# Performance work log

Measured on AMD Instinct MI355X. Metric: run time of the kernel, lower is better.

The kernel has to match this reference:

```python
import jax, jax.numpy as jnp
import numpy as np

D_MODEL = 1024
NUM_HEADS = 16
D_HEAD = D_MODEL // NUM_HEADS
B, S = 2, 2048


def setup_inputs() -> dict:
    key = jax.random.key(0)
    ks = jax.random.split(key, 12)
    s = 0.02
    return {
        "query": jax.random.normal(ks[0], (B, S, D_MODEL), jnp.float32),
        "key": jax.random.normal(ks[1], (B, S, D_MODEL), jnp.float32),
        "value": jax.random.normal(ks[2], (B, S, D_MODEL), jnp.float32),
        "mask": jnp.ones((B, 1, 1, S), jnp.float32),
        "W_q": jax.random.normal(ks[3], (D_MODEL, D_MODEL), jnp.float32) * s,
        "b_q": jnp.zeros((D_MODEL,), jnp.float32),
        "W_k": jax.random.normal(ks[4], (D_MODEL, D_MODEL), jnp.float32) * s,
        "b_k": jnp.zeros((D_MODEL,), jnp.float32),
        "W_v": jax.random.normal(ks[5], (D_MODEL, D_MODEL), jnp.float32) * s,
        "b_v": jnp.zeros((D_MODEL,), jnp.float32),
        "W_o": jax.random.normal(ks[6], (D_MODEL, D_MODEL), jnp.float32) * s,
        "b_o": jnp.zeros((D_MODEL,), jnp.float32),
    }


def reference(query, key, value, mask, W_q, b_q, W_k, b_k, W_v, b_v, W_o, b_o):
    # Linear projections (torch nn.Linear: x @ W.T + b; here W stored as [in, out])
    q = query @ W_q + b_q
    k = key @ W_k + b_k
    v = value @ W_v + b_v
    # [B, S, D] -> [B, H, S, Dh]
    def split_heads(x):
        b, s, _ = x.shape
        return x.reshape(b, s, NUM_HEADS, D_HEAD).transpose(0, 2, 1, 3)
    q, k, v = split_heads(q), split_heads(k), split_heads(v)
    # scaled dot-product attention; full [B,H,Sq,Sk] matrix (faithful to source)
    logits = jnp.einsum("bhqd,bhkd->bhqk", q, k) / jnp.sqrt(jnp.float32(D_HEAD))
    logits = logits + (1.0 - mask) * (-1e9)
    attn = jax.nn.softmax(logits, axis=-1)
    # dropout is identity in eval mode
    ctx = jnp.einsum("bhqk,bhkd->bhqd", attn, v)
    ctx = ctx.transpose(0, 2, 1, 3).reshape(ctx.shape[0], -1, D_MODEL)
    out = ctx @ W_o + b_o
    return out, attn
```

## Files before the change

kernel.cpp:

```cpp
#include <hip/hip_runtime.h>
#include <hip/hip_bf16.h>

#define BATCH 2
#define SEQ 2048
#define DM 1024
#define NH 16
#define DH 64
#define MTOT (BATCH*SEQ)

typedef __attribute__((ext_vector_type(8))) short bf16x8;
typedef __attribute__((ext_vector_type(4))) float f32x4;
typedef __attribute__((ext_vector_type(16))) float f32x16;
typedef __attribute__((ext_vector_type(4))) float float4v;
typedef __attribute__((ext_vector_type(8))) unsigned short u16x8;
typedef __attribute__((ext_vector_type(4))) unsigned short u16x4;

#define GLDS16(g, l) __builtin_amdgcn_global_load_lds(                         \
    (const __attribute__((address_space(1))) void*)(g),                        \
    (__attribute__((address_space(3))) void*)(l), 16, 0, 0)

static __device__ __forceinline__ float bf2f(unsigned short u) {
    unsigned int x = ((unsigned int)u) << 16;
    float f; __builtin_memcpy(&f, &x, 4); return f;
}
static __device__ __forceinline__ unsigned short f2bf(float f) {
    unsigned int x; __builtin_memcpy(&x, &f, 4);
    x += 0x7fffu + ((x >> 16) & 1);
    return (unsigned short)(x >> 16);
}
static __device__ __forceinline__ unsigned int cvt_pk_bf16(float a, float b) {
    unsigned int r;
    asm volatile("v_cvt_pk_bf16_f32 %0, %1, %2" : "=v"(r) : "v"(a), "v"(b));
    return r;
}

__global__ __launch_bounds__(256) void cvt_kernel(
    const float* __restrict__ q, const float* __restrict__ k, const float* __restrict__ v,
    unsigned short* __restrict__ oq, unsigned short* __restrict__ ok_, unsigned short* __restrict__ ov) {
    const float* in = blockIdx.y == 0 ? q : (blockIdx.y == 1 ? k : v);
    unsigned short* out = blockIdx.y == 0 ? oq : (blockIdx.y == 1 ? ok_ : ov);
    size_t i = ((size_t)blockIdx.x * 256 + threadIdx.x) * 8;
    float4v a = *(const float4v*)(in + i);
    float4v b = *(const float4v*)(in + i + 4);
    u16x8 r;
    r[0]=f2bf(a[0]); r[1]=f2bf(a[1]); r[2]=f2bf(a[2]); r[3]=f2bf(a[3]);
    r[4]=f2bf(b[0]); r[5]=f2bf(b[1]); r[6]=f2bf(b[2]); r[7]=f2bf(b[3]);
    *(u16x8*)(out + i) = r;
}

__global__ __launch_bounds__(256) void wtrans_kernel(
    const float* __restrict__ w0, const float* __restrict__ w1,
    const float* __restrict__ w2, const float* __restrict__ w3,
    unsigned short* __restrict__ t0, unsigned short* __restrict__ t1,
    unsigned short* __restrict__ t2, unsigned short* __restrict__ t3) {
    const float* w = blockIdx.z==0 ? w0 : blockIdx.z==1 ? w1 : blockIdx.z==2 ? w2 : w3;
    unsigned short* wt = blockIdx.z==0 ? t0 : blockIdx.z==1 ? t1 : blockIdx.z==2 ? t2 : t3;
    __shared__ float tile[64][65];
    const int t = threadIdx.x;
    const int k0 = blockIdx.x * 64, n0 = blockIdx.y * 64;
    const int tr = t >> 4, tc = t & 15;
#pragma unroll
    for (int i = 0; i < 4; ++i) {
        float4v val = *(const float4v*)(w + (size_t)(k0 + tr + 16*i) * DM + n0 + tc*4);
        tile[tr + 16*i][tc*4 + 0] = val[0];
        tile[tr + 16*i][tc*4 + 1] = val[1];
        tile[tr + 16*i][tc*4 + 2] = val[2];
        tile[tr + 16*i][tc*4 + 3] = val[3];
    }
    __syncthreads();
#pragma unroll
    for (int i = 0; i < 4; ++i) {
        u16x4 o;
#pragma unroll
        for (int j = 0; j < 4; ++j) o[j] = f2bf(tile[tc*4 + j][tr + 16*i]);
        *(u16x4*)(wt + (size_t)(n0 + tr + 16*i) * DM + k0 + tc*4) = o;
    }
}

__global__ __launch_bounds__(256) void vtrans_kernel(
    const unsigned short* __restrict__ vws, unsigned short* __restrict__ vtg) {
    __shared__ unsigned short tile[64][72];
    const int t = threadIdx.x;
    const int bh = blockIdx.y, b = bh >> 4, h = bh & 15;
    const int k0 = blockIdx.x * 64;
#pragma unroll
    for (int i = 0; i < 2; ++i) {
        int u = i*256 + t;
        int key = u >> 3, dc = (u & 7) * 8;
        u16x8 v = *(const u16x8*)(vws + (size_t)(b*SEQ + k0 + key)*DM + h*DH + dc);
#pragma unroll
        for (int j = 0; j < 8; ++j) tile[dc + j][key] = v[j];
    }
    __syncthreads();
#pragma unroll
    for (int i = 0; i < 2; ++i) {
        int u = i*256 + t;
        int d = u >> 3, kc = (u & 7) * 8;
        u16x8 o;
#pragma unroll
        for (int j = 0; j < 8; ++j) o[j] = tile[d][kc + j];
        *(u16x8*)(vtg + ((size_t)bh*DH + d)*SEQ + k0 + kc) = o;
    }
}

template<int OUTMODE>
static __device__ __forceinline__ void gemm_body(
    const unsigned short* __restrict__ A, const unsigned short* __restrict__ Bt,
    const float* __restrict__ bias, void* __restrict__ Cout,
    unsigned short* a_lds, unsigned short* b_lds) {
    constexpr int BM = 128, BN = 64, BK = 64, NT = DM / BK;
    const int tid = threadIdx.x;
    const int m0 = blockIdx.y * BM, n0 = blockIdx.x * BN;
    const int w = tid >> 6, l = tid & 63;
    const int lr = l & 15, lg = l >> 4;
    const int wm = (w >> 1) * 64, wn = (w & 1) * 32;
    f32x4 acc[4][2] = {};

    auto stage = [&](int buf, int kt) {
        const int k0 = kt * BK;
#pragma unroll
        for (int i = 0; i < 4; ++i) {
            int u = i*256 + tid;
            int row = u >> 3, slot = u & 7;
            int sc = (slot ^ (row & 7)) * 8;
            GLDS16(A + (size_t)(m0 + row)*DM + k0 + sc, a_lds + buf*BM*BK + u*8);
        }
#pragma unroll
        for (int i = 0; i < 2; ++i) {
            int u = i*256 + tid;
            int row = u >> 3, slot = u & 7;
            int sc = (slot ^ (row & 7)) * 8;
            GLDS16(Bt + (size_t)(n0 + row)*DM + k0 + sc, b_lds + buf*BN*BK + u*8);
        }
    };

    stage(0, 0);
    for (int kt = 0; kt < NT; ++kt) {
        __syncthreads();
        if (kt < NT-1) stage((kt+1)&1, kt+1);
        const char* ab = (const char*)(a_lds + (kt&1)*BM*BK);
        const char* bb = (const char*)(b_lds + (kt&1)*BN*BK);
        bf16x8 af[4][2], bfr[2][2];
#pragma unroll
        for (int r = 0; r < 4; ++r)
#pragma unroll
            for (int kc = 0; kc < 2; ++kc) {
                int row = wm + r*16 + lr;
                af[r][kc] = *(const bf16x8*)(ab + row*128 + ((kc*64 + lg*16) ^ ((row&7)<<4)));
            }
#pragma unroll
        for (int c = 0; c < 2; ++c)
#pragma unroll
            for (int kc = 0; kc < 2; ++kc) {
                int row = wn + c*16 + lr;
                bfr[c][kc] = *(const bf16x8*)(bb + row*128 + ((kc*64 + lg*16) ^ ((row&7)<<4)));
            }
#pragma unroll
        for (int r = 0; r < 4; ++r)
#pragma unroll
            for (int c = 0; c < 2; ++c)
#pragma unroll
                for (int kc = 0; kc < 2; ++kc)
                    acc[r][c] = __builtin_amdgcn_mfma_f32_16x16x32_bf16(af[r][kc], bfr[c][kc], acc[r][c], 0, 0, 0);
    }

#pragma unroll
    for (int r = 0; r < 4; ++r)
#pragma unroll
        for (int c = 0; c < 2; ++c) {
            int m = m0 + wm + r*16 + lg*4;
            int n = n0 + wn + c*16 + lr;
            float bb = bias[n];
            if constexpr (OUTMODE == 1) {
                float* o = (float*)Cout;
#pragma unroll
                for (int j = 0; j < 4; ++j) o[(size_t)(m+j)*DM + n] = acc[r][c][j] + bb;
            } else {
                unsigned short* o = (unsigned short*)Cout;
#pragma unroll
                for (int j = 0; j < 4; ++j) o[(size_t)(m+j)*DM + n] = f2bf(acc[r][c][j] + bb);
            }
        }
}

__global__ __launch_bounds__(256) void gemm_qkv_kernel(
    const unsigned short* __restrict__ A0, const unsigned short* __restrict__ A1, const unsigned short* __restrict__ A2,
    const unsigned short* __restrict__ B0, const unsigned short* __restrict__ B1, const unsigned short* __restrict__ B2,
    const float* __restrict__ c0, const float* __restrict__ c1, const float* __restrict__ c2,
    unsigned short* __restrict__ O0, unsigned short* __restrict__ O1, unsigned short* __restrict__ O2) {
    __shared__ __align__(16) unsigned short smem[2*128*64 + 2*64*64];
    const int z = blockIdx.z;
    const unsigned short* A = z==0 ? A0 : z==1 ? A1 : A2;
    const unsigned short* B = z==0 ? B0 : z==1 ? B1 : B2;
    const float* c = z==0 ? c0 : z==1 ? c1 : c2;
    unsigned short* O = z==0 ? O0 : z==1 ? O1 : O2;
    gemm_body<0>(A, B, c, O, smem, smem + 2*128*64);
}

__global__ __launch_bounds__(256) void gemm_out_kernel(
    const unsigned short* __restrict__ A, const unsigned short* __restrict__ Bt,
    const float* __restrict__ bias, float* __restrict__ Cout) {
    __shared__ __align__(16) unsigned short smem[2*128*64 + 2*64*64];
    gemm_body<1>(A, Bt, bias, Cout, smem, smem + 2*128*64);
}

__global__ __launch_bounds__(256) void attn_kernel(
    const unsigned short* __restrict__ qw, const unsigned short* __restrict__ kw,
    const unsigned short* __restrict__ vtg, const float* __restrict__ mask,
    float* __restrict__ attn_out, unsigned short* __restrict__ ctx) {
    constexpr int QB = 128, KB = 64, NT = SEQ / KB;
    __shared__ __align__(16) unsigned short smem[2*KB*DH + 2*KB*DH];
    unsigned short* kbuf = smem;
    unsigned short* vbuf = smem + 2*KB*DH;
    const int tid = threadIdx.x, w = tid >> 6, l = tid & 63;
    const int q32 = l & 31, hi = l >> 5;
    const int u0 = (blockIdx.x & 7) * 64 + (blockIdx.x >> 3);
    const int qblk = u0 & 15, bh = u0 >> 4;
    const int b = bh >> 4, h = bh & 15;
    const int q0 = qblk * QB;
    const int q = q0 + w*32 + q32;

    bf16x8 qf[4];
    {
        const unsigned short* qp = qw + ((size_t)(b*SEQ + q))*DM + h*DH + hi*8;
#pragma unroll
        for (int ks = 0; ks < 4; ++ks) {
            bf16x8 t = *(const bf16x8*)(qp + ks*16);
#pragma unroll
            for (int j = 0; j < 8; ++j) t[j] = (short)f2bf(bf2f((unsigned short)t[j]) * 0.125f);
            qf[ks] = t;
        }
    }

    auto stageK = [&](int buf, int kt) {
        const unsigned short* base = kw + ((size_t)(b*SEQ + kt*KB))*DM + h*DH;
#pragma unroll
        for (int i = 0; i < 2; ++i) {
            int uu = i*256 + tid;
            int row = uu >> 3, slot = uu & 7;
            int sc = (slot ^ (row & 7)) * 8;
            GLDS16(base + (size_t)row*DM + sc, kbuf + buf*KB*DH + uu*8);
        }
    };
    auto stageV = [&](int buf, int kt) {
        const unsigned short* base = vtg + ((size_t)bh*DH)*SEQ + (size_t)kt*KB;
#pragma unroll
        for (int i = 0; i < 2; ++i) {
            int uu = i*256 + tid;
            int row = uu >> 3, slot = uu & 7;
            int sc = (slot ^ (row & 7)) * 8;
            GLDS16(base + (size_t)row*SEQ + sc, vbuf + buf*KB*DH + uu*8);
        }
    };

    const float* mrow = mask + (size_t)b*SEQ;

    float rs = 0.f;
    stageK(0, 0);
    for (int kt = 0; kt < NT; ++kt) {
        __syncthreads();
        if (kt < NT-1) stageK((kt+1)&1, kt+1);
        const char* kb = (const char*)(kbuf + (kt&1)*KB*DH);
#pragma unroll
        for (int sub = 0; sub < 2; ++sub) {
            f32x16 s = {};
#pragma unroll
            for (int ks = 0; ks < 4; ++ks) {
                int key = sub*32 + q32;
                bf16x8 kf = *(const bf16x8*)(kb + key*128 + ((ks*32 + hi*16) ^ ((key&7)<<4)));
                s = __builtin_amdgcn_mfma_f32_32x32x16_bf16(kf, qf[ks], s, 0, 0, 0);
            }
#pragma unroll
            for (int rq = 0; rq < 4; ++rq) {
                float4v m4 = *(const float4v*)(mrow + kt*KB + sub*32 + rq*8 + hi*4);
#pragma unroll
                for (int r = 0; r < 4; ++r)
                    rs += __expf(s[rq*4 + r] + (1.0f - m4[r]) * (-1e9f));
            }
        }
    }
    rs += __shfl_xor(rs, 32);
    const float rinv = 1.0f / rs;

    f32x16 oacc[2] = {};
    float* attn_row = attn_out + ((size_t)bh*SEQ + q)*SEQ;
    stageK(0, 0); stageV(0, 0);
    for (int kt = 0; kt < NT; ++kt) {
        __syncthreads();
        if (kt < NT-1) { stageK((kt+1)&1, kt+1); stageV((kt+1)&1, kt+1); }
        const char* kb = (const char*)(kbuf + (kt&1)*KB*DH);
        const char* vb = (const char*)(vbuf + (kt&1)*KB*DH);
#pragma unroll
        for (int sub = 0; sub < 2; ++sub) {
            f32x16 s = {};
#pragma unroll
            for (int ks = 0; ks < 4; ++ks) {
                int key = sub*32 + q32;
                bf16x8 kf = *(const bf16x8*)(kb + key*128 + ((ks*32 + hi*16) ^ ((key&7)<<4)));
                s = __builtin_amdgcn_mfma_f32_32x32x16_bf16(kf, qf[ks], s, 0, 0, 0);
            }
            float p[16];
#pragma unroll
            for (int rq = 0; rq < 4; ++rq) {
                float4v m4 = *(const float4v*)(mrow + kt*KB + sub*32 + rq*8 + hi*4);
                float4v pv;
#pragma unroll
                for (int r = 0; r < 4; ++r) {
                    pv[r] = __expf(s[rq*4 + r] + (1.0f - m4[r]) * (-1e9f)) * rinv;
                    p[rq*4 + r] = pv[r];
                }
                *(float4v*)(attn_row + kt*KB + sub*32 + rq*8 + hi*4) = pv;
            }
#pragma unroll
            for (int half = 0; half < 2; ++half) {
                unsigned int w0 = cvt_pk_bf16(p[half*8+0], p[half*8+1]);
                unsigned int w1 = cvt_pk_bf16(p[half*8+2], p[half*8+3]);
                unsigned int w2 = cvt_pk_bf16(p[half*8+4], p[half*8+5]);
                unsigned int w3 = cvt_pk_bf16(p[half*8+6], p[half*8+7]);
                asm volatile("v_permlane32_swap_b32 %0, %1" : "+v"(w0), "+v"(w2));
                asm volatile("v_permlane32_swap_b32 %0, %1" : "+v"(w1), "+v"(w3));
                union { unsigned int uu[4]; bf16x8 v; } pa;
                pa.uu[0] = w0; pa.uu[1] = w1; pa.uu[2] = w2; pa.uu[3] = w3;
                const int ks4 = sub*2 + half;
#pragma unroll
                for (int dsub = 0; dsub < 2; ++dsub) {
                    int d = dsub*32 + q32;
                    bf16x8 vf = *(const bf16x8*)(vb + d*128 + ((ks4*32 + hi*16) ^ ((d&7)<<4)));
                    oacc[dsub] = __builtin_amdgcn_mfma_f32_32x32x16_bf16(pa.v, vf, oacc[dsub], 0, 0, 0);
                }
            }
        }
    }
#pragma unroll
    for (int dsub = 0; dsub < 2; ++dsub) {
        int d = h*DH + dsub*32 + q32;
#pragma unroll
        for (int reg = 0; reg < 16; ++reg) {
            int qr = q0 + w*32 + (reg&3) + 8*(reg>>2) + 4*hi;
            ctx[(size_t)(b*SEQ + qr)*DM + d] = f2bf(oacc[dsub][reg]);
        }
    }
}

extern "C" void kernel_launch(void* const* d_in, const int* in_sizes, int n_in,
                              void* d_out, int out_size, void* d_ws, size_t ws_size,
                              hipStream_t stream) {
    const float* query = (const float*)d_in[0];
    const float* key_  = (const float*)d_in[1];
    const float* value = (const float*)d_in[2];
    const float* mask  = (const float*)d_in[3];
    const float* W_q = (const float*)d_in[4];
    const float* b_q = (const float*)d_in[5];
    const float* W_k = (const float*)d_in[6];
    const float* b_k = (const float*)d_in[7];
    const float* W_v = (const float*)d_in[8];
    const float* b_v = (const float*)d_in[9];
    const float* W_o = (const float*)d_in[10];
    const float* b_o = (const float*)d_in[11];

    char* ws = (char*)d_ws;
    const size_t SZ = (size_t)MTOT * DM * 2;
    unsigned short* xq  = (unsigned short*)(ws);
    unsigned short* xk  = (unsigned short*)(ws + SZ);
    unsigned short* xv  = (unsigned short*)(ws + 2*SZ);
    unsigned short* wtq = (unsigned short*)(ws + 3*SZ);
    unsigned short* wtk = wtq + (size_t)DM*DM;
    unsigned short* wtv = wtk + (size_t)DM*DM;
    unsigned short* wto = wtv + (size_t)DM*DM;
    unsigned short* qws = (unsigned short*)(ws + 4*SZ);
    unsigned short* kws = (unsigned short*)(ws + 5*SZ);
    unsigned short* vws = (unsigned short*)(ws + 6*SZ);
    unsigned short* ctx = (unsigned short*)(ws + 7*SZ);
    unsigned short* vtg = xq;
    float* out_f  = (float*)d_out;
    float* attn_f = out_f + (size_t)MTOT * DM;

    cvt_kernel<<<dim3(MTOT*DM/(256*8), 3), 256, 0, stream>>>(query, key_, value, xq, xk, xv);
    wtrans_kernel<<<dim3(16, 16, 4), 256, 0, stream>>>(W_q, W_k, W_v, W_o, wtq, wtk, wtv, wto);
    gemm_qkv_kernel<<<dim3(16, 32, 3), 256, 0, stream>>>(xq, xk, xv, wtq, wtk, wtv,
                                                         b_q, b_k, b_v, qws, kws, vws);
    vtrans_kernel<<<dim3(SEQ/64, BATCH*NH), 256, 0, stream>>>(vws, vtg);
    attn_kernel<<<dim3(512), 256, 0, stream>>>(qws, kws, vtg, mask, attn_f, ctx);
    gemm_out_kernel<<<dim3(16, 32), 256, 0, stream>>>(ctx, wto, b_o, out_f);
}
```

Measured before the change: 305.0 us.

## Merge prep kernels, fuse V transpose into GEMM, split-K attention across warps

Merges the input conversion and weight transpose into one prep kernel. The V projection GEMM now writes its output directly in transposed per-head layout, which removes the separate vtrans pass. GEMM tiles grow from 128x64 to 128x128. The attention kernel doubles its threads to 512 so two warp groups each handle half of the key range, then combine row sums and context partials through shared memory. The aim is fewer launches, less memory traffic and more parallelism per block, at the cost of extra barriers and scattered 8-byte transposed stores.

```diff
diff --git a/kernel.cpp b/kernel.cpp
--- a/kernel.cpp
+++ b/kernel.cpp
@@ -34,72 +34,49 @@
     return r;
 }
 
-__global__ __launch_bounds__(256) void cvt_kernel(
+__global__ __launch_bounds__(256) void prep_kernel(
     const float* __restrict__ q, const float* __restrict__ k, const float* __restrict__ v,
-    unsigned short* __restrict__ oq, unsigned short* __restrict__ ok_, unsigned short* __restrict__ ov) {
-    const float* in = blockIdx.y == 0 ? q : (blockIdx.y == 1 ? k : v);
-    unsigned short* out = blockIdx.y == 0 ? oq : (blockIdx.y == 1 ? ok_ : ov);
-    size_t i = ((size_t)blockIdx.x * 256 + threadIdx.x) * 8;
-    float4v a = *(const float4v*)(in + i);
-    float4v b = *(const float4v*)(in + i + 4);
-    u16x8 r;
-    r[0]=f2bf(a[0]); r[1]=f2bf(a[1]); r[2]=f2bf(a[2]); r[3]=f2bf(a[3]);
-    r[4]=f2bf(b[0]); r[5]=f2bf(b[1]); r[6]=f2bf(b[2]); r[7]=f2bf(b[3]);
-    *(u16x8*)(out + i) = r;
-}
-
-__global__ __launch_bounds__(256) void wtrans_kernel(
+    unsigned short* __restrict__ oq, unsigned short* __restrict__ ok_, unsigned short* __restrict__ ov,
     const float* __restrict__ w0, const float* __restrict__ w1,
     const float* __restrict__ w2, const float* __restrict__ w3,
     unsigned short* __restrict__ t0, unsigned short* __restrict__ t1,
     unsigned short* __restrict__ t2, unsigned short* __restrict__ t3) {
-    const float* w = blockIdx.z==0 ? w0 : blockIdx.z==1 ? w1 : blockIdx.z==2 ? w2 : w3;
-    unsigned short* wt = blockIdx.z==0 ? t0 : blockIdx.z==1 ? t1 : blockIdx.z==2 ? t2 : t3;
     __shared__ float tile[64][65];
-    const int t = threadIdx.x;
-    const int k0 = blockIdx.x * 64, n0 = blockIdx.y * 64;
-    const int tr = t >> 4, tc = t & 15;
-#pragma unroll
-    for (int i = 0; i < 4; ++i) {
-        float4v val = *(const float4v*)(w + (size_t)(k0 + tr + 16*i) * DM + n0 + tc*4);
-        tile[tr + 16*i][tc*4 + 0] = val[0];
-        tile[tr + 16*i][tc*4 + 1] = val[1];
-        tile[tr + 16*i][tc*4 + 2] = val[2];
-        tile[tr + 16*i][tc*4 + 3] = val[3];
-    }
-    __syncthreads();
-#pragma unroll
-    for (int i = 0; i < 4; ++i) {
-        u16x4 o;
-#pragma unroll
-        for (int j = 0; j < 4; ++j) o[j] = f2bf(tile[tc*4 + j][tr + 16*i]);
-        *(u16x4*)(wt + (size_t)(n0 + tr + 16*i) * DM + k0 + tc*4) = o;
-    }
-}
-
-__global__ __launch_bounds__(256) void vtrans_kernel(
-    const unsigned short* __restrict__ vws, unsigned short* __restrict__ vtg) {
-    __shared__ unsigned short tile[64][72];
-    const int t = threadIdx.x;
-    const int bh = blockIdx.y, b = bh >> 4, h = bh & 15;
-    const int k0 = blockIdx.x * 64;
-#pragma unroll
-    for (int i = 0; i < 2; ++i) {
-        int u = i*256 + t;
-        int key = u >> 3, dc = (u & 7) * 8;
-        u16x8 v = *(const u16x8*)(vws + (size_t)(b*SEQ + k0 + key)*DM + h*DH + dc);
-#pragma unroll
-        for (int j = 0; j < 8; ++j) tile[dc + j][key] = v[j];
-    }
-    __syncthreads();
-#pragma unroll
-    for (int i = 0; i < 2; ++i) {
-        int u = i*256 + t;
-        int d = u >> 3, kc = (u & 7) * 8;
-        u16x8 o;
-#pragma unroll
-        for (int j = 0; j < 8; ++j) o[j] = tile[d][kc + j];
-        *(u16x8*)(vtg + ((size_t)bh*DH + d)*SEQ + k0 + kc) = o;
+    const int bx = blockIdx.x, t = threadIdx.x;
+    if (bx < 6144) {
+        const int slab = bx >> 11, bxr = bx & 2047;
+        const float* in = slab == 0 ? q : (slab == 1 ? k : v);
+        unsigned short* out = slab == 0 ? oq : (slab == 1 ? ok_ : ov);
+        size_t i = ((size_t)bxr * 256 + t) * 8;
+        float4v a = *(const float4v*)(in + i);
+        float4v b = *(const float4v*)(in + i + 4);
+        u16x8 r;
+        r[0]=f2bf(a[0]); r[1]=f2bf(a[1]); r[2]=f2bf(a[2]); r[3]=f2bf(a[3]);
+        r[4]=f2bf(b[0]); r[5]=f2bf(b[1]); r[6]=f2bf(b[2]); r[7]=f2bf(b[3]);
+        *(u16x8*)(out + i) = r;
+    } else {
+        const int i2 = bx - 6144;
+        const int z = i2 >> 8, rem = i2 & 255;
+        const float* w = z==0 ? w0 : z==1 ? w1 : z==2 ? w2 : w3;
+        unsigned short* wt = z==0 ? t0 : z==1 ? t1 : z==2 ? t2 : t3;
+        const int k0 = (rem & 15) * 64, n0 = (rem >> 4) * 64;
+        const int tr = t >> 4, tc = t & 15;
+#pragma unroll
+        for (int i = 0; i < 4; ++i) {
+            float4v val = *(const float4v*)(w + (size_t)(k0 + tr + 16*i) * DM + n0 + tc*4);
+            tile[tr + 16*i][tc*4 + 0] = val[0];
+            tile[tr + 16*i][tc*4 + 1] = val[1];
+            tile[tr + 16*i][tc*4 + 2] = val[2];
+            tile[tr + 16*i][tc*4 + 3] = val[3];
+        }
+        __syncthreads();
+#pragma unroll
+        for (int i = 0; i < 4; ++i) {
+            u16x4 o;
+#pragma unroll
+            for (int j = 0; j < 4; ++j) o[j] = f2bf(tile[tc*4 + j][tr + 16*i]);
+            *(u16x4*)(wt + (size_t)(n0 + tr + 16*i) * DM + k0 + tc*4) = o;
+        }
     }
 }
 
@@ -108,13 +85,13 @@
     const unsigned short* __restrict__ A, const unsigned short* __restrict__ Bt,
     const float* __restrict__ bias, void* __restrict__ Cout,
     unsigned short* a_lds, unsigned short* b_lds) {
-    constexpr int BM = 128, BN = 64, BK = 64, NT = DM / BK;
+    constexpr int BM = 128, BN = 128, BK = 64, NT = DM / BK;
     const int tid = threadIdx.x;
     const int m0 = blockIdx.y * BM, n0 = blockIdx.x * BN;
     const int w = tid >> 6, l = tid & 63;
     const int lr = l & 15, lg = l >> 4;
-    const int wm = (w >> 1) * 64, wn = (w & 1) * 32;
-    f32x4 acc[4][2] = {};
+    const int wm = (w >> 1) * 64, wn = (w & 1) * 64;
+    f32x4 acc[4][4] = {};
 
     auto stage = [&](int buf, int kt) {
         const int k0 = kt * BK;
@@ -126,7 +103,7 @@
             GLDS16(A + (size_t)(m0 + row)*DM + k0 + sc, a_lds + buf*BM*BK + u*8);
         }
 #pragma unroll
-        for (int i = 0; i < 2; ++i) {
+        for (int i = 0; i < 4; ++i) {
             int u = i*256 + tid;
             int row = u >> 3, slot = u & 7;
             int sc = (slot ^ (row & 7)) * 8;
@@ -140,7 +117,7 @@
         if (kt < NT-1) stage((kt+1)&1, kt+1);
         const char* ab = (const char*)(a_lds + (kt&1)*BM*BK);
         const char* bb = (const char*)(b_lds + (kt&1)*BN*BK);
-        bf16x8 af[4][2], bfr[2][2];
+        bf16x8 af[4][2], bfr[4][2];
 #pragma unroll
         for (int r = 0; r < 4; ++r)
 #pragma unroll
@@ -149,7 +126,7 @@
                 af[r][kc] = *(const bf16x8*)(ab + row*128 + ((kc*64 + lg*16) ^ ((row&7)<<4)));
             }
 #pragma unroll
-        for (int c = 0; c < 2; ++c)
+        for (int c = 0; c < 4; ++c)
 #pragma unroll
             for (int kc = 0; kc < 2; ++kc) {
                 int row = wn + c*16 + lr;
@@ -158,7 +135,7 @@
 #pragma unroll
         for (int r = 0; r < 4; ++r)
 #pragma unroll
-            for (int c = 0; c < 2; ++c)
+            for (int c = 0; c < 4; ++c)
 #pragma unroll
                 for (int kc = 0; kc < 2; ++kc)
                     acc[r][c] = __builtin_amdgcn_mfma_f32_16x16x32_bf16(af[r][kc], bfr[c][kc], acc[r][c], 0, 0, 0);
@@ -167,7 +144,7 @@
 #pragma unroll
     for (int r = 0; r < 4; ++r)
 #pragma unroll
-        for (int c = 0; c < 2; ++c) {
+        for (int c = 0; c < 4; ++c) {
             int m = m0 + wm + r*16 + lg*4;
             int n = n0 + wn + c*16 + lr;
             float bb = bias[n];
@@ -175,10 +152,18 @@
                 float* o = (float*)Cout;
 #pragma unroll
                 for (int j = 0; j < 4; ++j) o[(size_t)(m+j)*DM + n] = acc[r][c][j] + bb;
+            } else if constexpr (OUTMODE == 0) {
+                unsigned short* o = (unsigned short*)Cout;
+#pragma unroll
+                for (int j = 0; j < 4; ++j) o[(size_t)(m+j)*DM + n] = f2bf(acc[r][c][j] + bb);
             } else {
                 unsigned short* o = (unsigned short*)Cout;
-#pragma unroll
-                for (int j = 0; j < 4; ++j) o[(size_t)(m+j)*DM + n] = f2bf(acc[r][c][j] + bb);
+                int bb_ = m >> 11, kk = m & (SEQ-1);
+                int bh = bb_ * NH + (n >> 6), d = n & 63;
+                u16x4 ov;
+#pragma unroll
+                for (int j = 0; j < 4; ++j) ov[j] = f2bf(acc[r][c][j] + bb);
+                *(u16x4*)(o + ((size_t)bh*DH + d)*SEQ + kk) = ov;
             }
         }
 }
@@ -188,37 +173,40 @@
     const unsigned short* __restrict__ B0, const unsigned short* __restrict__ B1, const unsigned short* __restrict__ B2,
     const float* __restrict__ c0, const float* __restrict__ c1, const float* __restrict__ c2,
     unsigned short* __restrict__ O0, unsigned short* __restrict__ O1, unsigned short* __restrict__ O2) {
-    __shared__ __align__(16) unsigned short smem[2*128*64 + 2*64*64];
+    __shared__ __align__(16) unsigned short smem[2*128*64 + 2*128*64];
     const int z = blockIdx.z;
     const unsigned short* A = z==0 ? A0 : z==1 ? A1 : A2;
     const unsigned short* B = z==0 ? B0 : z==1 ? B1 : B2;
     const float* c = z==0 ? c0 : z==1 ? c1 : c2;
     unsigned short* O = z==0 ? O0 : z==1 ? O1 : O2;
-    gemm_body<0>(A, B, c, O, smem, smem + 2*128*64);
+    if (z == 2) gemm_body<2>(A, B, c, O, smem, smem + 2*128*64);
+    else        gemm_body<0>(A, B, c, O, smem, smem + 2*128*64);
 }
 
 __global__ __launch_bounds__(256) void gemm_out_kernel(
     const unsigned short* __restrict__ A, const unsigned short* __restrict__ Bt,
     const float* __restrict__ bias, float* __restrict__ Cout) {
-    __shared__ __align__(16) unsigned short smem[2*128*64 + 2*64*64];
+    __shared__ __align__(16) unsigned short smem[2*128*64 + 2*128*64];
     gemm_body<1>(A, Bt, bias, Cout, smem, smem + 2*128*64);
 }
 
-__global__ __launch_bounds__(256) void attn_kernel(
+__global__ __launch_bounds__(512) void attn_kernel(
     const unsigned short* __restrict__ qw, const unsigned short* __restrict__ kw,
     const unsigned short* __restrict__ vtg, const float* __restrict__ mask,
     float* __restrict__ attn_out, unsigned short* __restrict__ ctx) {
-    constexpr int QB = 128, KB = 64, NT = SEQ / KB;
-    __shared__ __align__(16) unsigned short smem[2*KB*DH + 2*KB*DH];
+    constexpr int QB = 128, KB = 64, NT2 = SEQ / KB / 2;
+    __shared__ __align__(16) unsigned short smem[2*2*KB*DH + 2*2*KB*DH];
     unsigned short* kbuf = smem;
-    unsigned short* vbuf = smem + 2*KB*DH;
+    unsigned short* vbuf = smem + 4*KB*DH;
     const int tid = threadIdx.x, w = tid >> 6, l = tid & 63;
+    const int hh = w >> 2, ws = w & 3;
     const int q32 = l & 31, hi = l >> 5;
     const int u0 = (blockIdx.x & 7) * 64 + (blockIdx.x >> 3);
     const int qblk = u0 & 15, bh = u0 >> 4;
     const int b = bh >> 4, h = bh & 15;
     const int q0 = qblk * QB;
-    const int q = q0 + w*32 + q32;
+    const int q = q0 + ws*32 + q32;
+    const int kbase = hh * (SEQ/2);
 
     bf16x8 qf[4];
     {
@@ -233,34 +221,32 @@
     }
 
     auto stageK = [&](int buf, int kt) {
-        const unsigned short* base = kw + ((size_t)(b*SEQ + kt*KB))*DM + h*DH;
-#pragma unroll
-        for (int i = 0; i < 2; ++i) {
-            int uu = i*256 + tid;
-            int row = uu >> 3, slot = uu & 7;
+#pragma unroll
+        for (int hf = 0; hf < 2; ++hf) {
+            int row = tid >> 3, slot = tid & 7;
             int sc = (slot ^ (row & 7)) * 8;
-            GLDS16(base + (size_t)row*DM + sc, kbuf + buf*KB*DH + uu*8);
+            const unsigned short* base = kw + ((size_t)(b*SEQ + hf*(SEQ/2) + kt*KB + row))*DM + h*DH;
+            GLDS16(base + sc, kbuf + (buf*2 + hf)*KB*DH + tid*8);
         }
     };
     auto stageV = [&](int buf, int kt) {
-        const unsigned short* base = vtg + ((size_t)bh*DH)*SEQ + (size_t)kt*KB;
-#pragma unroll
-        for (int i = 0; i < 2; ++i) {
-            int uu = i*256 + tid;
-            int row = uu >> 3, slot = uu & 7;
+#pragma unroll
+        for (int hf = 0; hf < 2; ++hf) {
+            int row = tid >> 3, slot = tid & 7;
             int sc = (slot ^ (row & 7)) * 8;
-            GLDS16(base + (size_t)row*SEQ + sc, vbuf + buf*KB*DH + uu*8);
+            const unsigned short* base = vtg + ((size_t)bh*DH + row)*SEQ + hf*(SEQ/2) + kt*KB;
+            GLDS16(base + sc, vbuf + (buf*2 + hf)*KB*DH + tid*8);
         }
     };
 
-    const float* mrow = mask + (size_t)b*SEQ;
+    const float* mrow = mask + (size_t)b*SEQ + kbase;
 
     float rs = 0.f;
     stageK(0, 0);
-    for (int kt = 0; kt < NT; ++kt) {
-        __syncthreads();
-        if (kt < NT-1) stageK((kt+1)&1, kt+1);
-        const char* kb = (const char*)(kbuf + (kt&1)*KB*DH);
+    for (int kt = 0; kt < NT2; ++kt) {
+        __syncthreads();
+        if (kt < NT2-1) stageK((kt+1)&1, kt+1);
+        const char* kb = (const char*)(kbuf + ((kt&1)*2 + hh)*KB*DH);
 #pragma unroll
         for (int sub = 0; sub < 2; ++sub) {
             f32x16 s = {};
@@ -280,16 +266,24 @@
         }
     }
     rs += __shfl_xor(rs, 32);
+    {
+        float* rbuf = (float*)smem;
+        __syncthreads();
+        rbuf[w*64 + l] = rs;
+        __syncthreads();
+        rs += rbuf[(w ^ 4)*64 + l];
+        __syncthreads();
+    }
     const float rinv = 1.0f / rs;
 
     f32x16 oacc[2] = {};
-    float* attn_row = attn_out + ((size_t)bh*SEQ + q)*SEQ;
+    float* attn_row = attn_out + ((size_t)bh*SEQ + q)*SEQ + kbase;
     stageK(0, 0); stageV(0, 0);
-    for (int kt = 0; kt < NT; ++kt) {
-        __syncthreads();
-        if (kt < NT-1) { stageK((kt+1)&1, kt+1); stageV((kt+1)&1, kt+1); }
-        const char* kb = (const char*)(kbuf + (kt&1)*KB*DH);
-        const char* vb = (const char*)(vbuf + (kt&1)*KB*DH);
+    for (int kt = 0; kt < NT2; ++kt) {
+        __syncthreads();
+        if (kt < NT2-1) { stageK((kt+1)&1, kt+1); stageV((kt+1)&1, kt+1); }
+        const char* kb = (const char*)(kbuf + ((kt&1)*2 + hh)*KB*DH);
+        const char* vb = (const char*)(vbuf + ((kt&1)*2 + hh)*KB*DH);
 #pragma unroll
         for (int sub = 0; sub < 2; ++sub) {
             f32x16 s = {};
@@ -331,13 +325,27 @@
             }
         }
     }
-#pragma unroll
-    for (int dsub = 0; dsub < 2; ++dsub) {
-        int d = h*DH + dsub*32 + q32;
-#pragma unroll
-        for (int reg = 0; reg < 16; ++reg) {
-            int qr = q0 + w*32 + (reg&3) + 8*(reg>>2) + 4*hi;
-            ctx[(size_t)(b*SEQ + qr)*DM + d] = f2bf(oacc[dsub][reg]);
+
+    float* cbuf = (float*)smem;
+    __syncthreads();
+    if (w >= 4) {
+        int base = ((w - 4)*64 + l) * 36;
+        *(f32x16*)(cbuf + base) = oacc[0];
+        *(f32x16*)(cbuf + base + 16) = oacc[1];
+    }
+    __syncthreads();
+    if (w < 4) {
+        int base = (w*64 + l) * 36;
+        oacc[0] += *(const f32x16*)(cbuf + base);
+        oacc[1] += *(const f32x16*)(cbuf + base + 16);
+#pragma unroll
+        for (int dsub = 0; dsub < 2; ++dsub) {
+            int d = h*DH + dsub*32 + q32;
+#pragma unroll
+            for (int reg = 0; reg < 16; ++reg) {
+                int qr = q0 + ws*32 + (reg&3) + 8*(reg>>2) + 4*hi;
+                ctx[(size_t)(b*SEQ + qr)*DM + d] = f2bf(oacc[dsub][reg]);
+            }
         }
     }
 }
@@ -369,17 +377,15 @@
     unsigned short* wto = wtv + (size_t)DM*DM;
     unsigned short* qws = (unsigned short*)(ws + 4*SZ);
     unsigned short* kws = (unsigned short*)(ws + 5*SZ);
-    unsigned short* vws = (unsigned short*)(ws + 6*SZ);
+    unsigned short* vtg = (unsigned short*)(ws + 6*SZ);
     unsigned short* ctx = (unsigned short*)(ws + 7*SZ);
-    unsigned short* vtg = xq;
     float* out_f  = (float*)d_out;
     float* attn_f = out_f + (size_t)MTOT * DM;
 
-    cvt_kernel<<<dim3(MTOT*DM/(256*8), 3), 256, 0, stream>>>(query, key_, value, xq, xk, xv);
-    wtrans_kernel<<<dim3(16, 16, 4), 256, 0, stream>>>(W_q, W_k, W_v, W_o, wtq, wtk, wtv, wto);
-    gemm_qkv_kernel<<<dim3(16, 32, 3), 256, 0, stream>>>(xq, xk, xv, wtq, wtk, wtv,
-                                                         b_q, b_k, b_v, qws, kws, vws);
-    vtrans_kernel<<<dim3(SEQ/64, BATCH*NH), 256, 0, stream>>>(vws, vtg);
-    attn_kernel<<<dim3(512), 256, 0, stream>>>(qws, kws, vtg, mask, attn_f, ctx);
-    gemm_out_kernel<<<dim3(16, 32), 256, 0, stream>>>(ctx, wto, b_o, out_f);
-}
+    prep_kernel<<<dim3(7168), 256, 0, stream>>>(query, key_, value, xq, xk, xv,
+                                                W_q, W_k, W_v, W_o, wtq, wtk, wtv, wto);
+    gemm_qkv_kernel<<<dim3(8, 32, 3), 256, 0, stream>>>(xq, xk, xv, wtq, wtk, wtv,
+                                                        b_q, b_k, b_v, qws, kws, vtg);
+    attn_kernel<<<dim3(512), 512, 0, stream>>>(qws, kws, vtg, mask, attn_f, ctx);
+    gemm_out_kernel<<<dim3(8, 32), 256, 0, stream>>>(ctx, wto, b_o, out_f);
+}
```

Measured after the change: 292.9 us. 4.0% less time.
